# Kernel optimization log

Hardware: AMD Instinct MI355X
Metric: run time of the kernel (lower is better)

Reference implementation:

```python
import jax, jax.numpy as jnp
from jax import lax
import numpy as np

B, N = 16, 4096
NPOINTS = [512, 64, 1]
NSAMPLE = [32, 64, 64]
RADIUS = [0.1, 0.2, 0.4]
SA_SPECS = [[9, 64, 128], [131, 128, 256], [259, 512, 1024]]  # use_xyz adds 3 to each input
CLS_SPEC = [1024, 1024, 512, 128]


def _mk(key, shape):
    return jax.random.normal(key, shape, jnp.float32) * 0.05


def setup_inputs() -> dict:
    key = jax.random.key(0)
    ks = iter(jax.random.split(key, 64))
    inp = {"pointcloud": jax.random.uniform(next(ks), (B, N, 9), jnp.float32)}
    # SA shared-MLP layers: 1x1 conv weight + folded eval-mode BN (scale g, bias b)
    for s, spec in enumerate(SA_SPECS):
        for l in range(len(spec) - 1):
            cin, cout = spec[l], spec[l + 1]
            inp[f"sa{s}w{l}"] = _mk(next(ks), (cout, cin))
            inp[f"sa{s}g{l}"] = jnp.ones((cout,), jnp.float32) + _mk(next(ks), (cout,))
            inp[f"sa{s}b{l}"] = _mk(next(ks), (cout,))
    for l in range(3):
        cin, cout = CLS_SPEC[l], CLS_SPEC[l + 1]
        inp[f"clsw{l}"] = _mk(next(ks), (cout, cin))
        inp[f"clsg{l}"] = jnp.ones((cout,), jnp.float32) + _mk(next(ks), (cout,))
        inp[f"clsb{l}"] = _mk(next(ks), (cout,))
    inp["clsw3"] = _mk(next(ks), (63, 128))
    inp["clsb3"] = _mk(next(ks), (63,))
    return inp


def fps(xyz, npoint):
    """Furthest point sampling. xyz: [B,N,3] -> indices [B,npoint]."""
    Bb, Nn, _ = xyz.shape

    def step(carry, _):
        dist, far = carry
        cen = jnp.take_along_axis(xyz, far[:, None, None], axis=1)  # [B,1,3]
        d = jnp.sum((xyz - cen) ** 2, -1)
        dist = jnp.minimum(dist, d)
        return (dist, jnp.argmax(dist, -1).astype(jnp.int32)), far

    init = (jnp.full((Bb, Nn), 1e10, xyz.dtype), jnp.zeros((Bb,), jnp.int32))
    _, idx = lax.scan(step, init, None, length=npoint)
    return jnp.transpose(idx)  # [B, npoint]


def ball_query(radius, K, xyz, new_xyz):
    """First-K-in-index-order neighbors within radius; pad with first hit (0 if none)."""
    Nn = xyz.shape[1]
    d2 = jnp.sum((new_xyz[:, :, None, :] - xyz[:, None, :, :]) ** 2, -1)  # [B,S,N]
    cand = jnp.where(d2 < radius * radius, jnp.arange(Nn, dtype=jnp.int32), Nn)
    vals = -lax.top_k(-cand, K)[0]  # K smallest candidate indices, ascending
    first = vals[..., :1]
    idx = jnp.where(vals >= Nn, first, vals)
    return jnp.where(idx >= Nn, 0, idx)


def sa_module(xyz, feats, npoint, radius, K, layers):
    s_idx = fps(xyz, npoint)
    new_xyz = jnp.take_along_axis(xyz, s_idx[:, :, None], axis=1)  # [B,S,3]
    idx = ball_query(radius, K, xyz, new_xyz)  # [B,S,K]
    gxyz = jax.vmap(lambda p, i: p[i])(xyz, idx) - new_xyz[:, :, None, :]  # [B,S,K,3]
    x = jnp.transpose(gxyz, (0, 3, 1, 2))  # [B,3,S,K]
    gf = jax.vmap(lambda f, i: f[:, i])(feats, idx)  # [B,C,S,K]
    x = jnp.concatenate([x, gf], axis=1)
    for (w, g, b) in layers:  # 1x1 conv + folded BN + ReLU
        x = jax.nn.relu(jnp.einsum('oc,bcsk->bosk', w, x) * g[:, None, None] + b[:, None, None])
    return new_xyz, jnp.max(x, axis=-1)  # max-pool over neighborhood -> [B,Cout,S]


def reference(pointcloud, sa0w0, sa0g0, sa0b0, sa0w1, sa0g1, sa0b1,
              sa1w0, sa1g0, sa1b0, sa1w1, sa1g1, sa1b1,
              sa2w0, sa2g0, sa2b0, sa2w1, sa2g1, sa2b1,
              clsw0, clsg0, clsb0, clsw1, clsg1, clsb1,
              clsw2, clsg2, clsb2, clsw3, clsb3):
    xyz = pointcloud[..., :3]
    feats = jnp.transpose(pointcloud[..., 3:], (0, 2, 1))  # [B,6,N]
    sa_params = [
        [(sa0w0, sa0g0, sa0b0), (sa0w1, sa0g1, sa0b1)],
        [(sa1w0, sa1g0, sa1b0), (sa1w1, sa1g1, sa1b1)],
        [(sa2w0, sa2g0, sa2b0), (sa2w1, sa2g1, sa2b1)],
    ]
    for k in range(3):
        xyz, feats = sa_module(xyz, feats, NPOINTS[k], RADIUS[k], NSAMPLE[k], sa_params[k])
    x = feats  # [B,1024,1]
    for (w, g, b) in [(clsw0, clsg0, clsb0), (clsw1, clsg1, clsb1), (clsw2, clsg2, clsb2)]:
        x = jax.nn.relu(jnp.einsum('oc,bcn->bon', w, x) * g[:, None] + b[:, None])
    return jnp.einsum('oc,bcn->bon', clsw3, x) + clsb3[:, None]  # [B,63,1]
```

## Files before the change

### kernel.cpp

```cpp
#include <hip/hip_runtime.h>

#define DEV __device__ __forceinline__

static constexpr int NB = 16;
static constexpr int N0 = 4096;

typedef float v2f __attribute__((ext_vector_type(2)));

DEV float nf_mul(float a, float b){ float r = a*b; asm volatile("" : "+v"(r)); return r; }
DEV float nf_add(float a, float b){ float r = a+b; asm volatile("" : "+v"(r)); return r; }
DEV float d2nf(float dx, float dy, float dz){
  return nf_add(nf_add(nf_mul(dx,dx), nf_mul(dy,dy)), nf_mul(dz,dz));
}

DEV v2f pk_sub(v2f a, v2f b){ v2f r; asm("v_pk_add_f32 %0, %1, %2 neg_lo:[0,1] neg_hi:[0,1]" : "=v"(r) : "v"(a), "v"(b)); return r; }
DEV v2f pk_mul(v2f a, v2f b){ v2f r; asm("v_pk_mul_f32 %0, %1, %2" : "=v"(r) : "v"(a), "v"(b)); return r; }
DEV v2f pk_add(v2f a, v2f b){ v2f r; asm("v_pk_add_f32 %0, %1, %2" : "=v"(r) : "v"(a), "v"(b)); return r; }
DEV v2f d2pk(v2f dx, v2f dy, v2f dz){
  return pk_add(pk_add(pk_mul(dx,dx), pk_mul(dy,dy)), pk_mul(dz,dz));
}

DEV float dpp_max63(float v){
  int o;
  o = __builtin_amdgcn_update_dpp(__float_as_int(v), __float_as_int(v), 0x118, 0xf, 0xf, false); v = fmaxf(v, __int_as_float(o));
  o = __builtin_amdgcn_update_dpp(__float_as_int(v), __float_as_int(v), 0x114, 0xf, 0xf, false); v = fmaxf(v, __int_as_float(o));
  o = __builtin_amdgcn_update_dpp(__float_as_int(v), __float_as_int(v), 0x112, 0xf, 0xf, false); v = fmaxf(v, __int_as_float(o));
  o = __builtin_amdgcn_update_dpp(__float_as_int(v), __float_as_int(v), 0x111, 0xf, 0xf, false); v = fmaxf(v, __int_as_float(o));
  o = __builtin_amdgcn_update_dpp(__float_as_int(v), __float_as_int(v), 0x142, 0xf, 0xf, false); v = fmaxf(v, __int_as_float(o));
  o = __builtin_amdgcn_update_dpp(__float_as_int(v), __float_as_int(v), 0x143, 0xf, 0xf, false); v = fmaxf(v, __int_as_float(o));
  return v;
}
DEV int dpp_min63(int v){
  int o;
  o = __builtin_amdgcn_update_dpp(v, v, 0x118, 0xf, 0xf, false); v = min(v, o);
  o = __builtin_amdgcn_update_dpp(v, v, 0x114, 0xf, 0xf, false); v = min(v, o);
  o = __builtin_amdgcn_update_dpp(v, v, 0x112, 0xf, 0xf, false); v = min(v, o);
  o = __builtin_amdgcn_update_dpp(v, v, 0x111, 0xf, 0xf, false); v = min(v, o);
  o = __builtin_amdgcn_update_dpp(v, v, 0x142, 0xf, 0xf, false); v = min(v, o);
  o = __builtin_amdgcn_update_dpp(v, v, 0x143, 0xf, 0xf, false); v = min(v, o);
  return v;
}

DEV void tr1(int i, const float* __restrict__ in, float* __restrict__ out, int C, int R){
  int r = i / C, c = i - r*C; out[(size_t)c*R + r] = in[i];
}

__global__ __launch_bounds__(256)
void k_front(const float* __restrict__ pc, float4* __restrict__ xyz,
             float4* __restrict__ nx0, float4* __restrict__ nx1,
             const float* __restrict__ w00, float* __restrict__ o00,
             const float* __restrict__ w01, float* __restrict__ o01,
             const float* __restrict__ w10, float* __restrict__ o10,
             const float* __restrict__ w11, float* __restrict__ o11,
             const float* __restrict__ w20, float* __restrict__ o20,
             const float* __restrict__ w21, float* __restrict__ o21)
{
  constexpr int N = 4096, NP = 512, NT = 256, NP2 = 64, NW = NT/64, NPR = N/(2*NT);
  if (blockIdx.x >= NB){
    int i = (int)(blockIdx.x - NB)*256 + threadIdx.x;
    if (i < 65536){
      const float* p = pc + (size_t)i*9;
      xyz[i] = make_float4(p[0], p[1], p[2], 0.f);
      return;
    }
    i -= 65536;
    if (i < 576)    { tr1(i, w00, o00, 9, 64);     return; } i -= 576;
    if (i < 8192)   { tr1(i, w01, o01, 64, 128);   return; } i -= 8192;
    if (i < 16768)  { tr1(i, w10, o10, 131, 128);  return; } i -= 16768;
    if (i < 32768)  { tr1(i, w11, o11, 128, 256);  return; } i -= 32768;
    if (i < 132608) { tr1(i, w20, o20, 259, 512);  return; } i -= 132608;
    if (i < 524288) { tr1(i, w21, o21, 512, 1024); return; }
    return;
  }
  __shared__ float sx[N], sy[N], sz[N];
  __shared__ float4 c1p[NP];
  __shared__ unsigned long long exch[2][NW];
  const int b = blockIdx.x, t = threadIdx.x, lane = t & 63, w = t >> 6;
  const float* src = pc + (size_t)b*N*9;
  v2f px[NPR], py[NPR], pz[NPR], pd[NPR];
  #pragma unroll
  for (int p=0;p<NPR;p++){
    int i0 = t + (2*p)*NT, i1 = i0 + NT;
    const float* a0 = src + (size_t)i0*9;
    const float* a1 = src + (size_t)i1*9;
    float x0=a0[0], y0=a0[1], z0=a0[2], x1=a1[0], y1=a1[1], z1=a1[2];
    v2f vx = {x0,x1}, vy = {y0,y1}, vz = {z0,z1}, vd = {1e10f,1e10f};
    px[p]=vx; py[p]=vy; pz[p]=vz; pd[p]=vd;
    sx[i0]=x0; sy[i0]=y0; sz[i0]=z0;
    sx[i1]=x1; sy[i1]=y1; sz[i1]=z1;
  }
  __syncthreads();
  float cx = sx[0], cy = sy[0], cz = sz[0];
  for (int it=0; it<NP; it++){
    if (t==0){
      nx0[(size_t)b*NP + it] = make_float4(cx,cy,cz,0.f);
      c1p[it] = make_float4(cx,cy,cz,0.f);
    }
    v2f cx2 = {cx,cx}, cy2 = {cy,cy}, cz2 = {cz,cz};
    float bv = -1.f; int bi = 0;
    #pragma unroll
    for (int p=0;p<NPR;p++){
      v2f d = d2pk(pk_sub(px[p],cx2), pk_sub(py[p],cy2), pk_sub(pz[p],cz2));
      float nx_ = fminf(pd[p].x, d.x);
      float ny_ = fminf(pd[p].y, d.y);
      pd[p].x = nx_; pd[p].y = ny_;
      if (nx_ > bv){ bv = nx_; bi = t + (2*p)*NT; }
      if (ny_ > bv){ bv = ny_; bi = t + (2*p+1)*NT; }
    }
    float gmv = dpp_max63(bv);
    float gm = __int_as_float(__builtin_amdgcn_readlane(__float_as_int(gmv), 63));
    int cand = (bv == gm) ? bi : 0x7fffffff;
    cand = dpp_min63(cand);
    if (lane == 63)
      exch[it&1][w] = ((unsigned long long)__float_as_uint(gm) << 32) | (unsigned)~cand;
    __syncthreads();
    unsigned long long g = exch[it&1][0];
    #pragma unroll
    for (int k=1;k<NW;k++){ unsigned long long e = exch[it&1][k]; if (e > g) g = e; }
    int far = (int)~(unsigned)g;
    cx = sx[far]; cy = sy[far]; cz = sz[far];
  }
  {
    float4 p0 = c1p[t], p1 = c1p[t + NT];
    v2f qx = {p0.x, p1.x}, qy = {p0.y, p1.y}, qz = {p0.z, p1.z}, qd = {1e10f, 1e10f};
    float4 a = c1p[0];
    for (int it=0; it<NP2; it++){
      if (t==0) nx1[(size_t)b*NP2 + it] = make_float4(a.x,a.y,a.z,0.f);
      v2f ax2 = {a.x,a.x}, ay2 = {a.y,a.y}, az2 = {a.z,a.z};
      v2f d = d2pk(pk_sub(qx,ax2), pk_sub(qy,ay2), pk_sub(qz,az2));
      float nx_ = fminf(qd.x, d.x);
      float ny_ = fminf(qd.y, d.y);
      qd.x = nx_; qd.y = ny_;
      float bv = nx_; int bi = t;
      if (ny_ > bv){ bv = ny_; bi = t + NT; }
      float gmv = dpp_max63(bv);
      float gm = __int_as_float(__builtin_amdgcn_readlane(__float_as_int(gmv), 63));
      int cand = (bv == gm) ? bi : 0x7fffffff;
      cand = dpp_min63(cand);
      if (lane == 63)
        exch[it&1][w] = ((unsigned long long)__float_as_uint(gm) << 32) | (unsigned)~cand;
      __syncthreads();
      unsigned long long g = exch[it&1][0];
      #pragma unroll
      for (int k=1;k<NW;k++){ unsigned long long e = exch[it&1][k]; if (e > g) g = e; }
      int far = (int)~(unsigned)g;
      float4 af = c1p[far];
      a = af;
    }
  }
}

__global__ __launch_bounds__(256)
void k_bq_all(const float4* __restrict__ xyz0, const float4* __restrict__ nx0,
              const float4* __restrict__ nx1,
              int* __restrict__ idx0, int* __restrict__ idx1, int* __restrict__ idx2)
{
  int wid = blockIdx.x*4 + (threadIdx.x >> 6);
  int lane = threadIdx.x & 63;
  const float4* xb; float4 c; int* o; int N, K; float r2;
  if (wid < 8192){
    int b = wid >> 9, s = wid & 511;
    xb = xyz0 + (size_t)b*4096; c = nx0[(size_t)b*512 + s];
    o = idx0 + ((size_t)b*512 + s)*32; N = 4096; K = 32; r2 = 0.01f;
  } else if (wid < 9216){
    int u = wid - 8192; int b = u >> 6, s = u & 63;
    xb = nx0 + (size_t)b*512; c = nx1[(size_t)b*64 + s];
    o = idx1 + ((size_t)b*64 + s)*64; N = 512; K = 64; r2 = 0.04f;
  } else {
    int b = wid - 9216;
    xb = nx1 + (size_t)b*64; c = nx1[(size_t)b*64];
    o = idx2 + (size_t)b*64; N = 64; K = 64; r2 = 0.16f;
  }
  int cnt = 0, first = 0;
  bool have_first = false;
  for (int base = 0; base < N; base += 64){
    float4 p = xb[base + lane];
    float d = d2nf(p.x - c.x, p.y - c.y, p.z - c.z);
    bool hit = (d <= r2);
    unsigned long long m = __ballot(hit);
    if (m){
      if (!have_first){ first = base + __ffsll((unsigned long long)m) - 1; have_first = true; }
      if (hit){
        int pos = cnt + __popcll(m & ((1ull << lane) - 1ull));
        if (pos < K) o[pos] = base + lane;
      }
      cnt += __popcll(m);
      if (cnt >= K) break;
    }
  }
  for (int pos = cnt + lane; pos < K; pos += 64) o[pos] = first;
}

__global__ __launch_bounds__(256)
void k_sa0(const float4* __restrict__ xyz, const float4* __restrict__ nx0,
           const int* __restrict__ idx0, const float* __restrict__ pc,
           const float* __restrict__ w0tg, const float* __restrict__ g0g, const float* __restrict__ b0g,
           const float* __restrict__ w1tg, const float* __restrict__ g1g, const float* __restrict__ b1g,
           float* __restrict__ f1)
{
  constexpr int K = 32, S = 512, C0 = 64, C1 = 128, G = 8;
  __shared__ float w1t[C0*C1];
  __shared__ float w0t[9*C0];
  __shared__ float gb0[2*C0];
  __shared__ float gb1[2*C1];
  __shared__ float xs[9][K];
  __shared__ float y0[C0][K];
  int t = threadIdx.x;
  for (int i=t;i<C0*C1;i+=256) w1t[i] = w1tg[i];
  for (int i=t;i<9*C0;i+=256)  w0t[i] = w0tg[i];
  if (t < C0){ gb0[t]=g0g[t]; gb0[C0+t]=b0g[t]; }
  if (t < C1){ gb1[t]=g1g[t]; gb1[C1+t]=b1g[t]; }
  int k0 = (t & 7)*4, og = t >> 3;
  for (int gi=0; gi<G; gi++){
    int gid = blockIdx.x*G + gi;
    int b = gid >> 9, s = gid & 511;
    __syncthreads();
    if (t < K){
      int i = idx0[(size_t)gid*K + t];
      float4 cen = nx0[(size_t)b*S + s];
      float4 p = xyz[(size_t)b*N0 + i];
      xs[0][t]=p.x-cen.x; xs[1][t]=p.y-cen.y; xs[2][t]=p.z-cen.z;
      const float* pr = pc + ((size_t)b*N0 + i)*9 + 3;
      #pragma unroll
      for (int f=0;f<6;f++) xs[3+f][t] = pr[f];
    }
    __syncthreads();
    float a0[2][4] = {};
    #pragma unroll
    for (int c=0;c<9;c++){
      float4 xv = *(const float4*)&xs[c][k0];
      #pragma unroll
      for (int j=0;j<2;j++){
        float w = w0t[c*C0 + og*2 + j];
        a0[j][0]+=w*xv.x; a0[j][1]+=w*xv.y; a0[j][2]+=w*xv.z; a0[j][3]+=w*xv.w;
      }
    }
    #pragma unroll
    for (int j=0;j<2;j++){
      int o = og*2 + j;
      float g = gb0[o], bb = gb0[C0+o];
      float4 r;
      r.x=fmaxf(a0[j][0]*g+bb,0.f); r.y=fmaxf(a0[j][1]*g+bb,0.f);
      r.z=fmaxf(a0[j][2]*g+bb,0.f); r.w=fmaxf(a0[j][3]*g+bb,0.f);
      *(float4*)&y0[o][k0] = r;
    }
    __syncthreads();
    float a1[4][4] = {};
    #pragma unroll 4
    for (int c=0;c<C0;c++){
      float4 yv = *(const float4*)&y0[c][k0];
      const float* wp = &w1t[c*C1 + og*4];
      #pragma unroll
      for (int j=0;j<4;j++){
        float w = wp[j];
        a1[j][0]+=w*yv.x; a1[j][1]+=w*yv.y; a1[j][2]+=w*yv.z; a1[j][3]+=w*yv.w;
      }
    }
    #pragma unroll
    for (int j=0;j<4;j++){
      int o = og*4 + j;
      float g = gb1[o], bb = gb1[C1+o];
      float m = fmaxf(fmaxf(a1[j][0]*g+bb, a1[j][1]*g+bb), fmaxf(a1[j][2]*g+bb, a1[j][3]*g+bb));
      m = fmaxf(m, 0.f);
      #pragma unroll
      for (int off=1; off<8; off<<=1) m = fmaxf(m, __shfl_xor(m, off));
      if ((t & 7) == 0) f1[((size_t)b*C1 + o)*S + s] = m;
    }
  }
}

__global__ __launch_bounds__(256)
void k_z1(const float* __restrict__ f1, const float* __restrict__ w0t, float* __restrict__ Z1)
{
  int b = blockIdx.z;
  int obase = blockIdx.x*64, ibase = blockIdx.y*64;
  int t = threadIdx.x;
  int i0 = ibase + (t & 15)*4, ol = (t >> 4)*4;
  float acc[4][4] = {};
  #pragma unroll 4
  for (int c=0;c<128;c++){
    float4 fv = *(const float4*)&f1[((size_t)b*128 + c)*512 + i0];
    float4 wv = *(const float4*)&w0t[(size_t)(3+c)*128 + obase + ol];
    float wa[4] = {wv.x, wv.y, wv.z, wv.w};
    float fa[4] = {fv.x, fv.y, fv.z, fv.w};
    #pragma unroll
    for (int j=0;j<4;j++)
      #pragma unroll
      for (int i=0;i<4;i++) acc[j][i] += wa[j]*fa[i];
  }
  #pragma unroll
  for (int j=0;j<4;j++)
    *(float4*)&Z1[((size_t)b*128 + obase + ol + j)*512 + i0] =
        make_float4(acc[j][0], acc[j][1], acc[j][2], acc[j][3]);
}

__global__ __launch_bounds__(256)
void k_sa1(const float4* __restrict__ nx0, const float4* __restrict__ nx1,
           const int* __restrict__ idx1, const float* __restrict__ Z1,
           const float* __restrict__ w0t, const float* __restrict__ g0, const float* __restrict__ b0,
           const float* __restrict__ w1t, const float* __restrict__ g1, const float* __restrict__ b1,
           float* __restrict__ f2)
{
  constexpr int K = 64, S = 64, C0 = 128, C1 = 256;
  __shared__ float y0[C0][K];
  __shared__ float gx[3][K];
  __shared__ int sidx[K];
  int gid = blockIdx.x, b = gid >> 6, s = gid & 63;
  int t = threadIdx.x;
  if (t < K) sidx[t] = idx1[(size_t)gid*K + t];
  __syncthreads();
  if (t < K){
    float4 cen = nx1[(size_t)b*S + s];
    float4 p = nx0[(size_t)b*512 + sidx[t]];
    gx[0][t]=p.x-cen.x; gx[1][t]=p.y-cen.y; gx[2][t]=p.z-cen.z;
  }
  __syncthreads();
  int k0 = (t & 15)*4, og = t >> 4;
  {
    float4 x0 = *(const float4*)&gx[0][k0];
    float4 x1 = *(const float4*)&gx[1][k0];
    float4 x2 = *(const float4*)&gx[2][k0];
    int i0=sidx[k0], i1=sidx[k0+1], i2=sidx[k0+2], i3=sidx[k0+3];
    #pragma unroll
    for (int j=0;j<8;j++){
      int o = og*8 + j;
      const float* zr = Z1 + ((size_t)b*C0 + o)*512;
      float wx=w0t[o], wy=w0t[C0+o], wz=w0t[2*C0+o];
      float g=g0[o], bb=b0[o];
      float4 r;
      r.x = fmaxf((zr[i0] + wx*x0.x + wy*x1.x + wz*x2.x)*g + bb, 0.f);
      r.y = fmaxf((zr[i1] + wx*x0.y + wy*x1.y + wz*x2.y)*g + bb, 0.f);
      r.z = fmaxf((zr[i2] + wx*x0.z + wy*x1.z + wz*x2.z)*g + bb, 0.f);
      r.w = fmaxf((zr[i3] + wx*x0.w + wy*x1.w + wz*x2.w)*g + bb, 0.f);
      *(float4*)&y0[o][k0] = r;
    }
  }
  __syncthreads();
  float a1[16][4] = {};
  #pragma unroll 2
  for (int c=0;c<C0;c++){
    float4 yv = *(const float4*)&y0[c][k0];
    const float* wp = &w1t[(size_t)c*C1 + og*16];
    #pragma unroll
    for (int j=0;j<16;j++){
      float w = wp[j];
      a1[j][0]+=w*yv.x; a1[j][1]+=w*yv.y; a1[j][2]+=w*yv.z; a1[j][3]+=w*yv.w;
    }
  }
  #pragma unroll
  for (int j=0;j<16;j++){
    int o = og*16 + j;
    float g=g1[o], bb=b1[o];
    float m = fmaxf(fmaxf(a1[j][0]*g+bb, a1[j][1]*g+bb), fmaxf(a1[j][2]*g+bb, a1[j][3]*g+bb));
    m = fmaxf(m, 0.f);
    #pragma unroll
    for (int off=1; off<16; off<<=1) m = fmaxf(m, __shfl_xor(m, off));
    if ((t & 15) == 0) f2[((size_t)b*C1 + o)*S + s] = m;
  }
}

__global__ __launch_bounds__(256)
void k_gather2(const float4* __restrict__ nx1, const int* __restrict__ idx2,
               const float* __restrict__ f2, float* __restrict__ x2)
{
  int b = blockIdx.x, t = threadIdx.x;
  __shared__ int sidx[64];
  if (t < 64) sidx[t] = idx2[b*64 + t];
  __syncthreads();
  float4 cen = nx1[(size_t)b*64];
  float* xo = x2 + (size_t)b*259*64;
  if (t < 64){
    float4 p = nx1[(size_t)b*64 + sidx[t]];
    xo[t] = p.x - cen.x; xo[64 + t] = p.y - cen.y; xo[128 + t] = p.z - cen.z;
  }
  for (int i=t; i<256*64; i+=256){
    int c = i >> 6, k = i & 63;
    xo[(3+c)*64 + k] = f2[((size_t)b*256 + c)*64 + sidx[k]];
  }
}

__global__ __launch_bounds__(256)
void k_sa2_l0(const float* __restrict__ x2, const float* __restrict__ w0t,
              const float* __restrict__ g0, const float* __restrict__ b0,
              float* __restrict__ y2)
{
  int b = blockIdx.y;
  int obase = blockIdx.x*64;
  int t = threadIdx.x;
  int k0 = (t & 15)*4, ol = (t >> 4)*4;
  const float* xb = x2 + (size_t)b*259*64;
  float acc[4][4] = {};
  #pragma unroll 4
  for (int c=0;c<259;c++){
    float4 xv = *(const float4*)&xb[c*64 + k0];
    float4 wv = *(const float4*)&w0t[(size_t)c*512 + obase + ol];
    float wa[4] = {wv.x, wv.y, wv.z, wv.w};
    float xa[4] = {xv.x, xv.y, xv.z, xv.w};
    #pragma unroll
    for (int j=0;j<4;j++)
      #pragma unroll
      for (int i=0;i<4;i++) acc[j][i] += wa[j]*xa[i];
  }
  #pragma unroll
  for (int j=0;j<4;j++){
    int o = obase + ol + j;
    float g = g0[o], bb = b0[o];
    float4 r;
    r.x=fmaxf(acc[j][0]*g+bb,0.f); r.y=fmaxf(acc[j][1]*g+bb,0.f);
    r.z=fmaxf(acc[j][2]*g+bb,0.f); r.w=fmaxf(acc[j][3]*g+bb,0.f);
    *(float4*)&y2[((size_t)b*512 + o)*64 + k0] = r;
  }
}

__global__ __launch_bounds__(256)
void k_sa2_l1(const float* __restrict__ y2, const float* __restrict__ w1t,
              const float* __restrict__ g1, const float* __restrict__ b1,
              float* __restrict__ f3)
{
  int b = blockIdx.y;
  int obase = blockIdx.x*64;
  int t = threadIdx.x;
  int k0 = (t & 15)*4, ol = (t >> 4)*4;
  const float* yb = y2 + (size_t)b*512*64;
  float acc[4][4] = {};
  #pragma unroll 4
  for (int c=0;c<512;c++){
    float4 yv = *(const float4*)&yb[c*64 + k0];
    float4 wv = *(const float4*)&w1t[(size_t)c*1024 + obase + ol];
    float wa[4] = {wv.x, wv.y, wv.z, wv.w};
    float ya[4] = {yv.x, yv.y, yv.z, yv.w};
    #pragma unroll
    for (int j=0;j<4;j++)
      #pragma unroll
      for (int i=0;i<4;i++) acc[j][i] += wa[j]*ya[i];
  }
  #pragma unroll
  for (int j=0;j<4;j++){
    int o = obase + ol + j;
    float g = g1[o], bb = b1[o];
    float m = fmaxf(fmaxf(acc[j][0]*g+bb, acc[j][1]*g+bb), fmaxf(acc[j][2]*g+bb, acc[j][3]*g+bb));
    m = fmaxf(m, 0.f);
    #pragma unroll
    for (int off=1; off<16; off<<=1) m = fmaxf(m, __shfl_xor(m, off));
    if ((t & 15) == 0) f3[(size_t)b*1024 + o] = m;
  }
}

template<bool RELU>
__global__ __launch_bounds__(256)
void k_lin(const float* __restrict__ x, const float* __restrict__ w,
           const float* __restrict__ g, const float* __restrict__ bb,
           float* __restrict__ y, int Cin, int Cout)
{
  __shared__ float xs[1024];
  int b = blockIdx.y, t = threadIdx.x;
  const float* xb = x + (size_t)b*Cin;
  for (int i=t;i<Cin;i+=256) xs[i] = xb[i];
  __syncthreads();
  int o = blockIdx.x*256 + t;
  if (o < Cout){
    const float4* wr = (const float4*)(w + (size_t)o*Cin);
    float acc = 0.f;
    #pragma unroll 8
    for (int c=0;c<Cin/4;c++){
      float4 wv = wr[c]; float4 xv = *(const float4*)&xs[c*4];
      acc += wv.x*xv.x + wv.y*xv.y + wv.z*xv.z + wv.w*xv.w;
    }
    float r;
    if (RELU) r = fmaxf(acc*g[o] + bb[o], 0.f);
    else      r = acc + bb[o];
    y[(size_t)b*Cout + o] = r;
  }
}

extern "C" void kernel_launch(void* const* d_in, const int* in_sizes, int n_in,
                              void* d_out, int out_size, void* d_ws, size_t ws_size,
                              hipStream_t stream)
{
  (void)in_sizes; (void)n_in; (void)out_size; (void)ws_size;
  const float* pc    = (const float*)d_in[0];
  const float* sa0w0 = (const float*)d_in[1];
  const float* sa0g0 = (const float*)d_in[2];
  const float* sa0b0 = (const float*)d_in[3];
  const float* sa0w1 = (const float*)d_in[4];
  const float* sa0g1 = (const float*)d_in[5];
  const float* sa0b1 = (const float*)d_in[6];
  const float* sa1w0 = (const float*)d_in[7];
  const float* sa1g0 = (const float*)d_in[8];
  const float* sa1b0 = (const float*)d_in[9];
  const float* sa1w1 = (const float*)d_in[10];
  const float* sa1g1 = (const float*)d_in[11];
  const float* sa1b1 = (const float*)d_in[12];
  const float* sa2w0 = (const float*)d_in[13];
  const float* sa2g0 = (const float*)d_in[14];
  const float* sa2b0 = (const float*)d_in[15];
  const float* sa2w1 = (const float*)d_in[16];
  const float* sa2g1 = (const float*)d_in[17];
  const float* sa2b1 = (const float*)d_in[18];
  const float* clsw0 = (const float*)d_in[19];
  const float* clsg0 = (const float*)d_in[20];
  const float* clsb0 = (const float*)d_in[21];
  const float* clsw1 = (const float*)d_in[22];
  const float* clsg1 = (const float*)d_in[23];
  const float* clsb1 = (const float*)d_in[24];
  const float* clsw2 = (const float*)d_in[25];
  const float* clsg2 = (const float*)d_in[26];
  const float* clsb2 = (const float*)d_in[27];
  const float* clsw3 = (const float*)d_in[28];
  const float* clsb3 = (const float*)d_in[29];

  char* ws = (char*)d_ws;
  size_t off = 0;
  auto A = [&](size_t bytes)->char* {
    char* p = ws + off;
    off = (off + bytes + 255) & ~(size_t)255;
    return p;
  };
  float4* xyz0 = (float4*)A((size_t)NB*N0*16);
  float4* nx0  = (float4*)A((size_t)NB*512*16);
  float4* nx1  = (float4*)A((size_t)NB*64*16);
  int*   idx0  = (int*)  A((size_t)NB*512*32*4);
  int*   idx1  = (int*)  A((size_t)NB*64*64*4);
  int*   idx2  = (int*)  A((size_t)NB*64*4);
  float* f1    = (float*)A((size_t)NB*128*512*4);
  float* Z1    = (float*)A((size_t)NB*128*512*4);
  float* f2    = (float*)A((size_t)NB*256*64*4);
  float* x2    = (float*)A((size_t)NB*259*64*4);
  float* y2    = (float*)A((size_t)NB*512*64*4);
  float* f3    = (float*)A((size_t)NB*1024*4);
  float* cb0   = (float*)A((size_t)NB*1024*4);
  float* cb1   = (float*)A((size_t)NB*512*4);
  float* cb2   = (float*)A((size_t)NB*128*4);
  float* w0t0  = (float*)A((size_t)9*64*4);
  float* w1t0  = (float*)A((size_t)64*128*4);
  float* w0t1  = (float*)A((size_t)131*128*4);
  float* w1t1  = (float*)A((size_t)128*256*4);
  float* w0t2  = (float*)A((size_t)259*512*4);
  float* w1t2  = (float*)A((size_t)512*1024*4);

  k_front<<<NB + 3050, 256, 0, stream>>>(pc, xyz0, nx0, nx1,
      sa0w0, w0t0, sa0w1, w1t0, sa1w0, w0t1, sa1w1, w1t1, sa2w0, w0t2, sa2w1, w1t2);

  k_bq_all<<<2308, 256, 0, stream>>>(xyz0, nx0, nx1, idx0, idx1, idx2);

  k_sa0<<<(NB*512)/8, 256, 0, stream>>>(xyz0, nx0, idx0, pc,
                                        w0t0, sa0g0, sa0b0, w1t0, sa0g1, sa0b1, f1);
  k_z1<<<dim3(2, 8, NB), 256, 0, stream>>>(f1, w0t1, Z1);
  k_sa1<<<NB*64, 256, 0, stream>>>(nx0, nx1, idx1, Z1,
                                   w0t1, sa1g0, sa1b0, w1t1, sa1g1, sa1b1, f2);
  k_gather2<<<NB, 256, 0, stream>>>(nx1, idx2, f2, x2);
  k_sa2_l0<<<dim3(8, NB), 256, 0, stream>>>(x2, w0t2, sa2g0, sa2b0, y2);
  k_sa2_l1<<<dim3(16, NB), 256, 0, stream>>>(y2, w1t2, sa2g1, sa2b1, f3);
  k_lin<true ><<<dim3(4, NB), 256, 0, stream>>>(f3,  clsw0, clsg0, clsb0, cb0, 1024, 1024);
  k_lin<true ><<<dim3(2, NB), 256, 0, stream>>>(cb0, clsw1, clsg1, clsb1, cb1, 1024, 512);
  k_lin<true ><<<dim3(1, NB), 256, 0, stream>>>(cb1, clsw2, clsg2, clsb2, cb2, 512, 128);
  k_lin<false><<<dim3(1, NB), 256, 0, stream>>>(cb2, clsw3, clsb3, clsb3, (float*)d_out, 128, 63);
}
```

Baseline: 861.2 us.

## Scalarize FPS loop, pass winner coords via LDS, fuse classifier MLP

The FPS inner loop goes from packed v2f arithmetic to scalar non-fused ops with predicated argmax, and each wave's winner now publishes its coordinates alongside the key. This removes the dependent shared-memory coordinate lookup after the barrier. The four classifier linear launches are merged into one kernel per batch that keeps activations in shared memory. That saves launches but leaves only 16 blocks streaming the large classifier weights.

```diff
diff --git a/kernel.cpp b/kernel.cpp
--- a/kernel.cpp
+++ b/kernel.cpp
@@ -4,20 +4,11 @@
 
 static constexpr int NB = 16;
 static constexpr int N0 = 4096;
-
-typedef float v2f __attribute__((ext_vector_type(2)));
 
 DEV float nf_mul(float a, float b){ float r = a*b; asm volatile("" : "+v"(r)); return r; }
 DEV float nf_add(float a, float b){ float r = a+b; asm volatile("" : "+v"(r)); return r; }
 DEV float d2nf(float dx, float dy, float dz){
   return nf_add(nf_add(nf_mul(dx,dx), nf_mul(dy,dy)), nf_mul(dz,dz));
-}
-
-DEV v2f pk_sub(v2f a, v2f b){ v2f r; asm("v_pk_add_f32 %0, %1, %2 neg_lo:[0,1] neg_hi:[0,1]" : "=v"(r) : "v"(a), "v"(b)); return r; }
-DEV v2f pk_mul(v2f a, v2f b){ v2f r; asm("v_pk_mul_f32 %0, %1, %2" : "=v"(r) : "v"(a), "v"(b)); return r; }
-DEV v2f pk_add(v2f a, v2f b){ v2f r; asm("v_pk_add_f32 %0, %1, %2" : "=v"(r) : "v"(a), "v"(b)); return r; }
-DEV v2f d2pk(v2f dx, v2f dy, v2f dz){
-  return pk_add(pk_add(pk_mul(dx,dx), pk_mul(dy,dy)), pk_mul(dz,dz));
 }
 
 DEV float dpp_max63(float v){
@@ -55,7 +46,7 @@
              const float* __restrict__ w20, float* __restrict__ o20,
              const float* __restrict__ w21, float* __restrict__ o21)
 {
-  constexpr int N = 4096, NP = 512, NT = 256, NP2 = 64, NW = NT/64, NPR = N/(2*NT);
+  constexpr int N = 4096, NP = 512, NT = 256, NP2 = 64, NW = NT/64, PT = N/NT;
   if (blockIdx.x >= NB){
     int i = (int)(blockIdx.x - NB)*256 + threadIdx.x;
     if (i < 65536){
@@ -74,20 +65,18 @@
   }
   __shared__ float sx[N], sy[N], sz[N];
   __shared__ float4 c1p[NP];
-  __shared__ unsigned long long exch[2][NW];
+  __shared__ unsigned long long xkey[2][NW];
+  __shared__ float xc[2][3][NW];
   const int b = blockIdx.x, t = threadIdx.x, lane = t & 63, w = t >> 6;
   const float* src = pc + (size_t)b*N*9;
-  v2f px[NPR], py[NPR], pz[NPR], pd[NPR];
+  float px[PT], py[PT], pz[PT], pd[PT];
   #pragma unroll
-  for (int p=0;p<NPR;p++){
-    int i0 = t + (2*p)*NT, i1 = i0 + NT;
-    const float* a0 = src + (size_t)i0*9;
-    const float* a1 = src + (size_t)i1*9;
-    float x0=a0[0], y0=a0[1], z0=a0[2], x1=a1[0], y1=a1[1], z1=a1[2];
-    v2f vx = {x0,x1}, vy = {y0,y1}, vz = {z0,z1}, vd = {1e10f,1e10f};
-    px[p]=vx; py[p]=vy; pz[p]=vz; pd[p]=vd;
-    sx[i0]=x0; sy[i0]=y0; sz[i0]=z0;
-    sx[i1]=x1; sy[i1]=y1; sz[i1]=z1;
+  for (int j=0;j<PT;j++){
+    int i = t + j*NT;
+    const float* a = src + (size_t)i*9;
+    float x=a[0], y=a[1], z=a[2];
+    px[j]=x; py[j]=y; pz[j]=z; pd[j]=1e10f;
+    sx[i]=x; sy[i]=y; sz[i]=z;
   }
   __syncthreads();
   float cx = sx[0], cy = sy[0], cz = sz[0];
@@ -96,56 +85,80 @@
       nx0[(size_t)b*NP + it] = make_float4(cx,cy,cz,0.f);
       c1p[it] = make_float4(cx,cy,cz,0.f);
     }
-    v2f cx2 = {cx,cx}, cy2 = {cy,cy}, cz2 = {cz,cz};
-    float bv = -1.f; int bi = 0;
-    #pragma unroll
-    for (int p=0;p<NPR;p++){
-      v2f d = d2pk(pk_sub(px[p],cx2), pk_sub(py[p],cy2), pk_sub(pz[p],cz2));
-      float nx_ = fminf(pd[p].x, d.x);
-      float ny_ = fminf(pd[p].y, d.y);
-      pd[p].x = nx_; pd[p].y = ny_;
-      if (nx_ > bv){ bv = nx_; bi = t + (2*p)*NT; }
-      if (ny_ > bv){ bv = ny_; bi = t + (2*p+1)*NT; }
+    float bv = -1.f; int bj = 0;
+    #pragma unroll
+    for (int j=0;j<PT;j++){
+      float d = d2nf(px[j]-cx, py[j]-cy, pz[j]-cz);
+      float nd = fminf(pd[j], d);
+      pd[j] = nd;
+      bool gt = nd > bv;
+      bv = gt ? nd : bv;
+      bj = gt ? j  : bj;
     }
     float gmv = dpp_max63(bv);
     float gm = __int_as_float(__builtin_amdgcn_readlane(__float_as_int(gmv), 63));
+    int bi = t + bj*NT;
     int cand = (bv == gm) ? bi : 0x7fffffff;
     cand = dpp_min63(cand);
-    if (lane == 63)
-      exch[it&1][w] = ((unsigned long long)__float_as_uint(gm) << 32) | (unsigned)~cand;
+    if (lane == 63){
+      int mi = cand;
+      xkey[it&1][w] = ((unsigned long long)__float_as_uint(gm) << 32) | (unsigned)~mi;
+      xc[it&1][0][w] = sx[mi]; xc[it&1][1][w] = sy[mi]; xc[it&1][2][w] = sz[mi];
+    }
     __syncthreads();
-    unsigned long long g = exch[it&1][0];
-    #pragma unroll
-    for (int k=1;k<NW;k++){ unsigned long long e = exch[it&1][k]; if (e > g) g = e; }
-    int far = (int)~(unsigned)g;
-    cx = sx[far]; cy = sy[far]; cz = sz[far];
+    {
+      int p = it&1;
+      unsigned long long kk = xkey[p][0];
+      float ax = xc[p][0][0], ay = xc[p][1][0], az = xc[p][2][0];
+      #pragma unroll
+      for (int q=1;q<NW;q++){
+        unsigned long long kq = xkey[p][q];
+        bool g = kq > kk;
+        kk = g ? kq : kk;
+        ax = g ? xc[p][0][q] : ax;
+        ay = g ? xc[p][1][q] : ay;
+        az = g ? xc[p][2][q] : az;
+      }
+      cx = ax; cy = ay; cz = az;
+    }
   }
   {
     float4 p0 = c1p[t], p1 = c1p[t + NT];
-    v2f qx = {p0.x, p1.x}, qy = {p0.y, p1.y}, qz = {p0.z, p1.z}, qd = {1e10f, 1e10f};
-    float4 a = c1p[0];
+    float qx0=p0.x, qy0=p0.y, qz0=p0.z, qd0=1e10f;
+    float qx1=p1.x, qy1=p1.y, qz1=p1.z, qd1=1e10f;
+    float ax = c1p[0].x, ay = c1p[0].y, az = c1p[0].z;
     for (int it=0; it<NP2; it++){
-      if (t==0) nx1[(size_t)b*NP2 + it] = make_float4(a.x,a.y,a.z,0.f);
-      v2f ax2 = {a.x,a.x}, ay2 = {a.y,a.y}, az2 = {a.z,a.z};
-      v2f d = d2pk(pk_sub(qx,ax2), pk_sub(qy,ay2), pk_sub(qz,az2));
-      float nx_ = fminf(qd.x, d.x);
-      float ny_ = fminf(qd.y, d.y);
-      qd.x = nx_; qd.y = ny_;
-      float bv = nx_; int bi = t;
-      if (ny_ > bv){ bv = ny_; bi = t + NT; }
+      if (t==0) nx1[(size_t)b*NP2 + it] = make_float4(ax,ay,az,0.f);
+      float d0 = d2nf(qx0-ax, qy0-ay, qz0-az);
+      float d1 = d2nf(qx1-ax, qy1-ay, qz1-az);
+      qd0 = fminf(qd0, d0);
+      qd1 = fminf(qd1, d1);
+      float bv = qd0; int bi = t;
+      if (qd1 > bv){ bv = qd1; bi = t + NT; }
       float gmv = dpp_max63(bv);
       float gm = __int_as_float(__builtin_amdgcn_readlane(__float_as_int(gmv), 63));
       int cand = (bv == gm) ? bi : 0x7fffffff;
       cand = dpp_min63(cand);
-      if (lane == 63)
-        exch[it&1][w] = ((unsigned long long)__float_as_uint(gm) << 32) | (unsigned)~cand;
+      if (lane == 63){
+        int mi = cand;
+        float4 pt = c1p[mi];
+        xkey[it&1][w] = ((unsigned long long)__float_as_uint(gm) << 32) | (unsigned)~mi;
+        xc[it&1][0][w] = pt.x; xc[it&1][1][w] = pt.y; xc[it&1][2][w] = pt.z;
+      }
       __syncthreads();
-      unsigned long long g = exch[it&1][0];
-      #pragma unroll
-      for (int k=1;k<NW;k++){ unsigned long long e = exch[it&1][k]; if (e > g) g = e; }
-      int far = (int)~(unsigned)g;
-      float4 af = c1p[far];
-      a = af;
+      int p = it&1;
+      unsigned long long kk = xkey[p][0];
+      float nax = xc[p][0][0], nay = xc[p][1][0], naz = xc[p][2][0];
+      #pragma unroll
+      for (int q=1;q<NW;q++){
+        unsigned long long kq = xkey[p][q];
+        bool g = kq > kk;
+        kk = g ? kq : kk;
+        nax = g ? xc[p][0][q] : nax;
+        nay = g ? xc[p][1][q] : nay;
+        naz = g ? xc[p][2][q] : naz;
+      }
+      ax = nax; ay = nay; az = naz;
     }
   }
 }
@@ -446,30 +459,60 @@
   }
 }
 
-template<bool RELU>
-__global__ __launch_bounds__(256)
-void k_lin(const float* __restrict__ x, const float* __restrict__ w,
-           const float* __restrict__ g, const float* __restrict__ bb,
-           float* __restrict__ y, int Cin, int Cout)
-{
-  __shared__ float xs[1024];
-  int b = blockIdx.y, t = threadIdx.x;
-  const float* xb = x + (size_t)b*Cin;
-  for (int i=t;i<Cin;i+=256) xs[i] = xb[i];
-  __syncthreads();
-  int o = blockIdx.x*256 + t;
-  if (o < Cout){
-    const float4* wr = (const float4*)(w + (size_t)o*Cin);
+__global__ __launch_bounds__(256)
+void k_cls(const float* __restrict__ f3,
+           const float* __restrict__ w0, const float* __restrict__ g0, const float* __restrict__ b0,
+           const float* __restrict__ w1, const float* __restrict__ g1, const float* __restrict__ b1,
+           const float* __restrict__ w2, const float* __restrict__ g2, const float* __restrict__ b2,
+           const float* __restrict__ w3, const float* __restrict__ b3,
+           float* __restrict__ out)
+{
+  __shared__ float xa[1024], xb[1024];
+  int b = blockIdx.x, t = threadIdx.x;
+  for (int i=t;i<1024;i+=256) xa[i] = f3[(size_t)b*1024 + i];
+  __syncthreads();
+  for (int o=t;o<1024;o+=256){
+    const float4* wr = (const float4*)(w0 + (size_t)o*1024);
     float acc = 0.f;
     #pragma unroll 8
-    for (int c=0;c<Cin/4;c++){
-      float4 wv = wr[c]; float4 xv = *(const float4*)&xs[c*4];
+    for (int c=0;c<256;c++){
+      float4 wv = wr[c]; float4 xv = *(const float4*)&xa[c*4];
       acc += wv.x*xv.x + wv.y*xv.y + wv.z*xv.z + wv.w*xv.w;
     }
-    float r;
-    if (RELU) r = fmaxf(acc*g[o] + bb[o], 0.f);
-    else      r = acc + bb[o];
-    y[(size_t)b*Cout + o] = r;
+    xb[o] = fmaxf(acc*g0[o] + b0[o], 0.f);
+  }
+  __syncthreads();
+  for (int o=t;o<512;o+=256){
+    const float4* wr = (const float4*)(w1 + (size_t)o*1024);
+    float acc = 0.f;
+    #pragma unroll 8
+    for (int c=0;c<256;c++){
+      float4 wv = wr[c]; float4 xv = *(const float4*)&xb[c*4];
+      acc += wv.x*xv.x + wv.y*xv.y + wv.z*xv.z + wv.w*xv.w;
+    }
+    xa[o] = fmaxf(acc*g1[o] + b1[o], 0.f);
+  }
+  __syncthreads();
+  if (t < 128){
+    const float4* wr = (const float4*)(w2 + (size_t)t*512);
+    float acc = 0.f;
+    #pragma unroll 8
+    for (int c=0;c<128;c++){
+      float4 wv = wr[c]; float4 xv = *(const float4*)&xa[c*4];
+      acc += wv.x*xv.x + wv.y*xv.y + wv.z*xv.z + wv.w*xv.w;
+    }
+    xb[t] = fmaxf(acc*g2[t] + b2[t], 0.f);
+  }
+  __syncthreads();
+  if (t < 63){
+    const float4* wr = (const float4*)(w3 + (size_t)t*128);
+    float acc = 0.f;
+    #pragma unroll
+    for (int c=0;c<32;c++){
+      float4 wv = wr[c]; float4 xv = *(const float4*)&xb[c*4];
+      acc += wv.x*xv.x + wv.y*xv.y + wv.z*xv.z + wv.w*xv.w;
+    }
+    out[(size_t)b*63 + t] = acc + b3[t];
   }
 }
 
@@ -528,9 +571,6 @@
   float* x2    = (float*)A((size_t)NB*259*64*4);
   float* y2    = (float*)A((size_t)NB*512*64*4);
   float* f3    = (float*)A((size_t)NB*1024*4);
-  float* cb0   = (float*)A((size_t)NB*1024*4);
-  float* cb1   = (float*)A((size_t)NB*512*4);
-  float* cb2   = (float*)A((size_t)NB*128*4);
   float* w0t0  = (float*)A((size_t)9*64*4);
   float* w1t0  = (float*)A((size_t)64*128*4);
   float* w0t1  = (float*)A((size_t)131*128*4);
@@ -551,8 +591,6 @@
   k_gather2<<<NB, 256, 0, stream>>>(nx1, idx2, f2, x2);
   k_sa2_l0<<<dim3(8, NB), 256, 0, stream>>>(x2, w0t2, sa2g0, sa2b0, y2);
   k_sa2_l1<<<dim3(16, NB), 256, 0, stream>>>(y2, w1t2, sa2g1, sa2b1, f3);
-  k_lin<true ><<<dim3(4, NB), 256, 0, stream>>>(f3,  clsw0, clsg0, clsb0, cb0, 1024, 1024);
-  k_lin<true ><<<dim3(2, NB), 256, 0, stream>>>(cb0, clsw1, clsg1, clsb1, cb1, 1024, 512);
-  k_lin<true ><<<dim3(1, NB), 256, 0, stream>>>(cb1, clsw2, clsg2, clsb2, cb2, 512, 128);
-  k_lin<false><<<dim3(1, NB), 256, 0, stream>>>(cb2, clsw3, clsb3, clsb3, (float*)d_out, 128, 63);
-}
+  k_cls<<<NB, 256, 0, stream>>>(f3, clsw0, clsg0, clsb0, clsw1, clsg1, clsb1,
+                                clsw2, clsg2, clsb2, clsw3, clsb3, (float*)d_out);
+}
```

Result: slower. 1.072 ms (+24.5%).
